# Kernel tuning notes

Measured on AMD Instinct MI355X. Metric: run time of the kernel, lower is better.

Reference implementation:

```python
import jax, jax.numpy as jnp
import numpy as np

# Dims: B INRs, N probe points, d_in=2 coords, hidden H, out D_OUT, proj P
B, N, D_IN, H, D_OUT, P = 128, 4096, 2, 128, 3, 128
W0_SIREN = 30.0  # SIREN frequency scale
LN_EPS = 1e-5


def setup_inputs() -> dict:
    key = jax.random.key(0)
    ks = jax.random.split(key, 12)
    sn = lambda k, shape, sc: (jax.random.normal(k, shape, dtype=jnp.float32) * sc)
    return {
        # per-sample SIREN params, torch layout: weight [b, in, out, 1], bias [b, out, 1]
        "w0": sn(ks[0], (B, D_IN, H, 1), 1.0 / D_IN),
        "w1": sn(ks[1], (B, H, H, 1), np.sqrt(6.0 / H) / W0_SIREN),
        "w2": sn(ks[2], (B, H, D_OUT, 1), np.sqrt(6.0 / H) / W0_SIREN),
        "b0": sn(ks[3], (B, H, 1), 0.1),
        "b1": sn(ks[4], (B, H, 1), 0.1),
        "b2": sn(ks[5], (B, D_OUT, 1), 0.1),
        # learned probe coordinates, initialized U[-1, 1) as in the module
        "inputs": jax.random.uniform(ks[6], (1, N, D_IN), dtype=jnp.float32, minval=-1.0, maxval=1.0),
        # projection (num_inputs -> proj_dim) + LayerNorm params, one per probed layer (4 total)
        "pw": sn(ks[7], (4, N, P), 1.0 / np.sqrt(N)),
        "pb": jnp.zeros((4, P), jnp.float32),
        "ln_g": jnp.ones((4, P), jnp.float32),
        "ln_b": jnp.zeros((4, P), jnp.float32),
    }


def _layernorm(x, g, b):
    m = jnp.mean(x, axis=-1, keepdims=True)
    v = jnp.mean(jnp.square(x - m), axis=-1, keepdims=True)
    return (x - m) * jax.lax.rsqrt(v + LN_EPS) * g + b


def reference(w0, w1, w2, b0, b1, b2, inputs, pw, pb, ln_g, ln_b):
    b = w0.shape[0]
    x = jnp.broadcast_to(inputs, (b,) + inputs.shape[1:])  # [b, n, d_in]

    def lin(h, W, bb):
        # per-sample linear: [b,n,i] @ [b,i,o] + [b,1,o]
        return jnp.einsum('bni,bio->bno', h, W[..., 0]) + bb[:, None, :, 0]

    h1 = jnp.sin(W0_SIREN * lin(x, w0, b0))   # [b, n, H]
    h2 = jnp.sin(W0_SIREN * lin(h1, w1, b1))  # [b, n, H]
    h3 = lin(h2, w2, b2)                      # [b, n, D_OUT] (last layer: no sine)
    feats = [x, h1, h2, h3]  # probe features per node layer (input coords + activations)

    outs = []
    for i, f in enumerate(feats):
        # permute to [b, dim_i, n], project n -> P, then LayerNorm over P
        z = jnp.einsum('bnd,np->bdp', f, pw[i]) + pb[i]
        outs.append(_layernorm(z, ln_g[i], ln_b[i]))
    return jnp.concatenate(outs, axis=1)  # [b, d_in + H + H + D_OUT, P]
```

## Files before the change

kernel.cpp:

```cpp
#include <hip/hip_runtime.h>
#include <hip/hip_bf16.h>


typedef unsigned short u16;
typedef __attribute__((ext_vector_type(8))) short short8;
typedef __attribute__((ext_vector_type(4))) short short4v;
typedef __attribute__((ext_vector_type(4))) float f32x4;
typedef __attribute__((ext_vector_type(4))) float float4v;

#define DEV __device__ __forceinline__

#define KSC 4.7746482927568605f

DEV float b2f(u16 h){ return __uint_as_float(((unsigned)h) << 16); }
DEV u16 f2b(float f){
  unsigned u = __float_as_uint(f);
  return (u16)((u + 0x7FFFu + ((u >> 16) & 1u)) >> 16);
}
DEV u16 f2b_hw(float f){
  __hip_bfloat16 h = __float2bfloat16(f);
  return __builtin_bit_cast(unsigned short, h);
}
DEV float sin_rev(float r){
#if __has_builtin(__builtin_amdgcn_sinf)
  return __builtin_amdgcn_sinf(r);
#else
  return __sinf(r * 6.283185307179586f);
#endif
}
template<int C> DEV float dpp_add(float x){
  int yi = __builtin_amdgcn_update_dpp(0, __float_as_int(x), C, 0xF, 0xF, true);
  return x + __int_as_float(yi);
}
DEV float sum16(float x){
  x = dpp_add<0x128>(x); x = dpp_add<0x124>(x);
  x = dpp_add<0x122>(x); x = dpp_add<0x121>(x);
  return x;
}

DEV int is_bf16_fmt(const void* lng){ return *(const unsigned*)lng == 0x3F803F80u; }
struct In {
  const float* f; const u16* h; int bf;
  DEV In(const void* p, int b_) : f((const float*)p), h((const u16*)p), bf(b_) {}
  DEV float at(size_t i) const { return bf ? b2f(h[i]) : f[i]; }
};

__global__ __launch_bounds__(256) void k_prep(const void* pwv, const void* inpv,
                                              const void* lngv,
                                              u16* __restrict__ pwT,
                                              float* __restrict__ xbuf){
  const int bf = is_bf16_fmt(lngv);
  const int t = threadIdx.x;
  if (blockIdx.x == 256){
    In inp(inpv, bf);
    for (int i = t; i < 8192; i += 256) xbuf[i] = inp.at(i);
    return;
  }
  In pw(pwv, bf);
  __shared__ u16 tile[64 * 129];
  const int layer = blockIdx.x >> 6;
  const int n0 = (blockIdx.x & 63) * 64;
  const size_t base = ((size_t)layer * 4096 + n0) * 128;
#pragma unroll
  for (int k = 0; k < 32; k++){
    int idx = k * 256 + t, n = idx >> 7, p = idx & 127;
    tile[n * 129 + p] = f2b(pw.at(base + (size_t)n * 128 + p));
  }
  __syncthreads();
  u16* dst = pwT + (size_t)layer * 128 * 4096 + n0;
#pragma unroll
  for (int k = 0; k < 32; k++){
    int idx = k * 256 + t, p = idx >> 6, n = idx & 63;
    dst[(size_t)p * 4096 + n] = tile[n * 129 + p];
  }
}

#define S_NK 136
#define S_T  40

template<bool PARTIAL>
__global__ __launch_bounds__(512, 2)
void k_main(const void* w0v, const void* w1v, const void* w2v,
            const void* b0v, const void* b1v, const void* b2v,
            const void* pbv, const void* lgv, const void* lbv,
            const u16* __restrict__ pwTg, const float* __restrict__ xbuf,
            float* __restrict__ outp, int TS){
  __shared__ __align__(16) u16 spw01[2][128 * S_T];
  __shared__ __align__(16) u16 spw23[2][2][128 * S_T];
  __shared__ __align__(16) u16 sh1nk[32 * S_NK];
  __shared__ __align__(16) u16 sh1T[128 * S_T];
  __shared__ __align__(16) u16 sh2T[2][128 * S_T];
  __shared__ __align__(16) u16 sxT[16 * S_T];
  __shared__ float sW2[512];
  __shared__ float sb2[4];
  __shared__ float sPB[512], sG[512], sBB[512];

  float* sP1 = (float*)sh1nk;
  float* sP2 = (float*)sh1T;
  float* sM  = (float*)sh2T;
  float* sI  = (float*)sh2T + 512;

  const int bf = is_bf16_fmt(lgv);
  In w0(w0v, bf), w1(w1v, bf), w2(w2v, bf), b0(b0v, bf), b1(b1v, bf),
     b2(b2v, bf), pb(pbv, bf), lg(lgv, bf), lb(lbv, bf);

  const int t = threadIdx.x;
  const int b = blockIdx.x & 127, sseg = blockIdx.x >> 7;
  const int lane = t & 63, wave = t >> 6, quad = lane >> 4, r16 = lane & 15;
  const int oo = wave * 16 + r16;

  if (t >= 256 && t < 384){
    int i = t - 256;
    sW2[i * 4 + 0] = w2.at(((size_t)b * 128 + i) * 3 + 0);
    sW2[i * 4 + 1] = w2.at(((size_t)b * 128 + i) * 3 + 1);
    sW2[i * 4 + 2] = w2.at(((size_t)b * 128 + i) * 3 + 2);
    sW2[i * 4 + 3] = 0.f;
  }
  if (t < 4) sb2[t] = (t < 3) ? b2.at(b * 3 + t) : 0.f;
  sPB[t] = pb.at(t); sG[t] = lg.at(t); sBB[t] = lb.at(t);
  for (int k = t; k < 16 * S_T; k += 512) sxT[k] = 0;

  const int p1n = t >> 4, p1hb = (t & 15) * 8;
  float w00[8], w01[8], b00[8];
#pragma unroll
  for (int j = 0; j < 8; j++){
    w00[j] = w0.at((size_t)b * 256 + p1hb + j) * KSC;
    w01[j] = w0.at((size_t)b * 256 + 128 + p1hb + j) * KSC;
    b00[j] = b0.at((size_t)b * 128 + p1hb + j) * KSC;
  }
  const int p2h = t & 127, p2nb = (t >> 7) * 8;
  const float q00 = w0.at((size_t)b * 256 + p2h) * KSC;
  const float q01 = w0.at((size_t)b * 256 + 128 + p2h) * KSC;
  const float qb0 = b0.at((size_t)b * 128 + p2h) * KSC;
  const float bias1k = b1.at((size_t)b * 128 + oo) * KSC;

  short8 w1f[4];
#pragma unroll
  for (int ks = 0; ks < 4; ks++){
#pragma unroll
    for (int j = 0; j < 8; j++)
      w1f[ks][j] = (short)f2b(w1.at((size_t)b * 16384 +
                                    (size_t)(ks * 32 + quad * 8 + j) * 128 + oo));
  }
  short8 a1s = {0,0,0,0,0,0,0,0};
  if (r16 == 0){
#pragma unroll
    for (int j = 0; j < 8; j++) a1s[j] = (short)0x3F80;
  }

  const int pwrow = t >> 2, pwc = t & 3;
  const u16* pwsrc = pwTg + (size_t)pwrow * 4096 + pwc * 8;
  const int pwdofs = pwrow * S_T + pwc * 8;
  const int bofs = oo * S_T + quad * 8;

  const f32x4 zz = {0.f,0.f,0.f,0.f};
  f32x4 az1[8], az2[8], ay[8], az0 = zz, az3 = zz;
#pragma unroll
  for (int i = 0; i < 8; i++){ az1[i] = zz; az2[i] = zz; ay[i] = zz; }

  const int n0first = sseg * TS * 32;
  short8 pwv[4];
#pragma unroll
  for (int L = 0; L < 4; L++)
    pwv[L] = *(const short8*)(pwsrc + (size_t)L * 524288 + n0first);
  float2 xp1 = *(const float2*)(xbuf + (size_t)(n0first + p1n) * 2);

  __syncthreads();

  int cb = 0;
  for (int nt = 0; nt < TS; nt++){
    const int n0 = (sseg * TS + nt) * 32;

    float4v xq[4];
#pragma unroll
    for (int q = 0; q < 4; q++)
      xq[q] = *(const float4v*)(xbuf + (size_t)(n0 + p2nb) * 2 + q * 4);
    *(short8*)&spw01[0][pwdofs] = pwv[0];
    *(short8*)&spw01[1][pwdofs] = pwv[1];
    *(short8*)&spw23[cb][0][pwdofs] = pwv[2];
    *(short8*)&spw23[cb][1][pwdofs] = pwv[3];
    if ((t & 15) == 0){
      sxT[p1n] = f2b(xp1.x);
      sxT[S_T + p1n] = f2b(xp1.y);
    }
    {
      short8 v;
#pragma unroll
      for (int j = 0; j < 8; j++){
        float a = fmaf(xp1.y, w01[j], fmaf(xp1.x, w00[j], b00[j]));
        a -= rintf(a);
        v[j] = (short)f2b_hw(sin_rev(a));
      }
      *(short8*)&sh1nk[p1n * S_NK + p1hb] = v;
    }
    {
      short8 v;
#pragma unroll
      for (int j = 0; j < 8; j++){
        float x0 = xq[j >> 1][(j & 1) * 2], x1 = xq[j >> 1][(j & 1) * 2 + 1];
        float a = fmaf(x1, q01, fmaf(x0, q00, qb0));
        a -= rintf(a);
        v[j] = (short)f2b_hw(sin_rev(a));
      }
      *(short8*)&sh1T[p2h * S_T + p2nb] = v;
    }
    if (nt){
      const u16* s2p  = sh2T[cb ^ 1];
      const short8 bb2 = *(const short8*)&spw23[cb ^ 1][0][bofs];
      const short8 bb3 = *(const short8*)&spw23[cb ^ 1][1][bofs];
#pragma unroll
      for (int mb = 0; mb < 8; mb++){
        short8 a = *(const short8*)&s2p[(mb * 16 + r16) * S_T + quad * 8];
        az2[mb] = __builtin_amdgcn_mfma_f32_16x16x32_bf16(a, bb2, az2[mb], 0, 0, 0);
        ay[mb]  = __builtin_amdgcn_mfma_f32_16x16x32_bf16(a, bb3, ay[mb], 0, 0, 0);
      }
    }
    __syncthreads();

    {
      const int nn = (nt + 1 < TS) ? nt + 1 : nt;
      const int n0n = (sseg * TS + nn) * 32;
      short8 pwn[4];
#pragma unroll
      for (int L = 0; L < 4; L++)
        pwn[L] = *(const short8*)(pwsrc + (size_t)L * 524288 + n0n);
      float2 xp1n = *(const float2*)(xbuf + (size_t)(n0n + p1n) * 2);

      f32x4 h0 = zz, h1a = zz;
#pragma unroll
      for (int ks = 0; ks < 4; ks++){
        h0  = __builtin_amdgcn_mfma_f32_16x16x32_bf16(
                *(short8*)&sh1nk[r16 * S_NK + ks * 32 + quad * 8], w1f[ks], h0, 0, 0, 0);
        h1a = __builtin_amdgcn_mfma_f32_16x16x32_bf16(
                *(short8*)&sh1nk[(16 + r16) * S_NK + ks * 32 + quad * 8], w1f[ks], h1a, 0, 0, 0);
      }
      az0 = __builtin_amdgcn_mfma_f32_16x16x32_bf16(
              *(short8*)&sxT[r16 * S_T + quad * 8], *(short8*)&spw01[0][bofs], az0, 0, 0, 0);
#pragma unroll
      for (int mb = 0; mb < 8; mb++)
        az1[mb] = __builtin_amdgcn_mfma_f32_16x16x32_bf16(
                    *(short8*)&sh1T[(mb * 16 + r16) * S_T + quad * 8],
                    *(short8*)&spw01[1][bofs], az1[mb], 0, 0, 0);
      az3 = __builtin_amdgcn_mfma_f32_16x16x32_bf16(a1s, *(short8*)&spw23[cb][1][bofs], az3, 0, 0, 0);
      {
        short4v v;
#pragma unroll
        for (int r = 0; r < 4; r++){
          float a = fmaf(h0[r], KSC, bias1k); a -= rintf(a);
          v[r] = (short)f2b_hw(sin_rev(a));
        }
        *(short4v*)&sh2T[cb][oo * S_T + quad * 4] = v;
#pragma unroll
        for (int r = 0; r < 4; r++){
          float a = fmaf(h1a[r], KSC, bias1k); a -= rintf(a);
          v[r] = (short)f2b_hw(sin_rev(a));
        }
        *(short4v*)&sh2T[cb][oo * S_T + 16 + quad * 4] = v;
      }

#pragma unroll
      for (int L = 0; L < 4; L++) pwv[L] = pwn[L];
      xp1 = xp1n;
    }
    __syncthreads();
    cb ^= 1;
  }

  {
    const u16* s2p  = sh2T[cb ^ 1];
    const short8 bb2 = *(const short8*)&spw23[cb ^ 1][0][bofs];
    const short8 bb3 = *(const short8*)&spw23[cb ^ 1][1][bofs];
#pragma unroll
    for (int mb = 0; mb < 8; mb++){
      short8 a = *(const short8*)&s2p[(mb * 16 + r16) * S_T + quad * 8];
      az2[mb] = __builtin_amdgcn_mfma_f32_16x16x32_bf16(a, bb2, az2[mb], 0, 0, 0);
      ay[mb]  = __builtin_amdgcn_mfma_f32_16x16x32_bf16(a, bb3, ay[mb], 0, 0, 0);
    }
  }

  const int p = oo;
  float S3 = (quad == 0) ? az3[0] : 0.f;
  S3 += __shfl_xor(S3, 16, 64); S3 += __shfl_xor(S3, 32, 64);
  float z3v[3];
#pragma unroll
  for (int d = 0; d < 3; d++){
    float a = 0.f;
#pragma unroll
    for (int mb = 0; mb < 8; mb++)
#pragma unroll
      for (int r = 0; r < 4; r++)
        a = fmaf(sW2[(mb * 16 + quad * 4 + r) * 4 + d], ay[mb][r], a);
    a += __shfl_xor(a, 16, 64); a += __shfl_xor(a, 32, 64);
    z3v[d] = a + sb2[d] * S3;
  }

  if (PARTIAL){
    float* zp = outp + ((size_t)(sseg * 128 + b)) * 261 * 128;
    if (quad == 0){
#pragma unroll
      for (int r = 0; r < 2; r++) zp[(size_t)r * 128 + p] = az0[r];
#pragma unroll
      for (int d = 0; d < 3; d++) zp[(size_t)(258 + d) * 128 + p] = z3v[d];
    }
#pragma unroll
    for (int mb = 0; mb < 8; mb++)
#pragma unroll
      for (int r = 0; r < 4; r++){
        int drow = mb * 16 + quad * 4 + r;
        zp[(size_t)(2 + drow) * 128 + p]   = az1[mb][r];
        zp[(size_t)(130 + drow) * 128 + p] = az2[mb][r];
      }
    return;
  }

  const float pb0v = sPB[p],       pb1v = sPB[128 + p];
  const float pb2v = sPB[256 + p], pb3v = sPB[384 + p];

  auto rowsum = [&](float v, int row, bool wr){
    float s1 = sum16(v), s2 = sum16(v * v);
    if (wr && r16 == 0){ sP1[row * 8 + wave] = s1; sP2[row * 8 + wave] = s2; }
  };
#pragma unroll
  for (int r = 0; r < 2; r++) rowsum(az0[r] + pb0v, r, quad == 0);
#pragma unroll
  for (int mb = 0; mb < 8; mb++)
#pragma unroll
    for (int r = 0; r < 4; r++)
      rowsum(az1[mb][r] + pb1v, 2 + mb * 16 + quad * 4 + r, true);
#pragma unroll
  for (int mb = 0; mb < 8; mb++)
#pragma unroll
    for (int r = 0; r < 4; r++)
      rowsum(az2[mb][r] + pb2v, 130 + mb * 16 + quad * 4 + r, true);
#pragma unroll
  for (int d = 0; d < 3; d++) rowsum(z3v[d] + pb3v, 258 + d, quad == 0);
  __syncthreads();

  if (t < 261){
    float s1 = 0.f, s2 = 0.f;
#pragma unroll
    for (int w = 0; w < 8; w++){ s1 += sP1[t * 8 + w]; s2 += sP2[t * 8 + w]; }
    float m = s1 * (1.f / 128.f);
    float var = fmaf(-m, m, s2 * (1.f / 128.f));
    sM[t] = m;
    sI[t] = rsqrtf(fmaxf(var, 0.f) + 1e-5f);
  }
  __syncthreads();

  const size_t ob = (size_t)b * 261 * 128;
  auto emit = [&](float v, int row, int grp){
    outp[ob + (size_t)row * 128 + p] =
      (v - sM[row]) * sI[row] * sG[grp * 128 + p] + sBB[grp * 128 + p];
  };
  if (quad == 0){
#pragma unroll
    for (int r = 0; r < 2; r++) emit(az0[r] + pb0v, r, 0);
#pragma unroll
    for (int d = 0; d < 3; d++) emit(z3v[d] + pb3v, 258 + d, 3);
  }
#pragma unroll
  for (int mb = 0; mb < 8; mb++)
#pragma unroll
    for (int r = 0; r < 4; r++)
      emit(az1[mb][r] + pb1v, 2 + mb * 16 + quad * 4 + r, 1);
#pragma unroll
  for (int mb = 0; mb < 8; mb++)
#pragma unroll
    for (int r = 0; r < 4; r++)
      emit(az2[mb][r] + pb2v, 130 + mb * 16 + quad * 4 + r, 2);
}

__global__ __launch_bounds__(256)
void k_ln(const float* __restrict__ zp, const void* pbv, const void* lgv,
          const void* lbv, float* __restrict__ out, int split){
  const int bf = is_bf16_fmt(lgv);
  In pb(pbv, bf), lg(lgv, bf), lb(lbv, bf);
  const int lane = threadIdx.x & 63;
  const int row = blockIdx.x * 4 + (threadIdx.x >> 6);
  const int b = row / 261, d = row % 261;
  const int grp = (d < 2) ? 0 : (d < 130) ? 1 : (d < 258) ? 2 : 3;
  const int p0 = lane * 2;
  float v0 = pb.at(grp * 128 + p0), v1 = pb.at(grp * 128 + p0 + 1);
  for (int s2 = 0; s2 < split; s2++){
    const float* zr = zp + ((size_t)(s2 * 128 + b) * 261 + d) * 128;
    v0 += zr[p0]; v1 += zr[p0 + 1];
  }
  float s1 = v0 + v1, s2s = v0 * v0 + v1 * v1;
#pragma unroll
  for (int o = 1; o < 64; o <<= 1){
    s1 += __shfl_xor(s1, o, 64);
    s2s += __shfl_xor(s2s, o, 64);
  }
  float m = s1 * (1.f / 128.f);
  float var = fmaf(-m, m, s2s * (1.f / 128.f));
  float inv = rsqrtf(fmaxf(var, 0.f) + 1e-5f);
  float2 o2;
  o2.x = (v0 - m) * inv * lg.at(grp * 128 + p0)     + lb.at(grp * 128 + p0);
  o2.y = (v1 - m) * inv * lg.at(grp * 128 + p0 + 1) + lb.at(grp * 128 + p0 + 1);
  *(float2*)(out + (size_t)row * 128 + p0) = o2;
}

extern "C" void kernel_launch(void* const* d_in, const int* in_sizes, int n_in,
                              void* d_out, int out_size, void* d_ws, size_t ws_size,
                              hipStream_t stream){
  const void* w0  = d_in[0];
  const void* w1  = d_in[1];
  const void* w2  = d_in[2];
  const void* b0  = d_in[3];
  const void* b1  = d_in[4];
  const void* b2  = d_in[5];
  const void* inp = d_in[6];
  const void* pw  = d_in[7];
  const void* pb  = d_in[8];
  const void* lng = d_in[9];
  const void* lnb = d_in[10];
  float* out = (float*)d_out;

  u16* pwT    = (u16*)d_ws;
  float* xbuf = (float*)((char*)d_ws + (size_t)4 * 128 * 4096 * 2);
  const size_t zoff = (size_t)4 * 128 * 4096 * 2 + 8192 * 4;
  float* zp = (float*)((char*)d_ws + zoff);
  const size_t seg = (size_t)128 * 261 * 128 * 4;

  const int split = (ws_size >= zoff + 2 * seg) ? 2 : 1;

  k_prep<<<257, 256, 0, stream>>>(pw, inp, lng, pwT, xbuf);
  if (split == 2){
    k_main<true><<<256, 512, 0, stream>>>(w0, w1, w2, b0, b1, b2,
        pb, lng, lnb, pwT, xbuf, zp, 64);
    k_ln<<<(128 * 261) / 4, 256, 0, stream>>>(zp, pb, lng, lnb, out, 2);
  } else {
    k_main<false><<<128, 512, 0, stream>>>(w0, w1, w2, b0, b1, b2,
        pb, lng, lnb, pwT, xbuf, out, 128);
  }
}
```

Baseline: 226.7 us.

## Hoist batch-independent input and bias-sum projections into a separate precompute kernel

The probe coordinates are shared across the batch, so the layer-0 projection x·pw[0] is the same for every sample. The new k_zs kernel computes it once, together with the column sums of pw[3] used by the last-layer bias. The main kernel no longer streams pw[0] or issues the x and bias MFMAs per tile, which cuts one of four pw load streams and some shared-memory traffic; the LN kernels then read the precomputed sums. In exchange, k_zs runs one thread per output column over a serial 4096-element reduction on only two blocks, and that latency-bound launch sits on the critical path.

Result: slower. 622.8 us (+174.7%).

```diff
diff --git a/kernel.cpp b/kernel.cpp
--- a/kernel.cpp
+++ b/kernel.cpp
@@ -75,6 +75,34 @@
   }
 }
 
+__global__ __launch_bounds__(256)
+void k_zs(const void* pwv, const void* inpv, const void* lngv,
+          float* __restrict__ zs){
+  const int bf = is_bf16_fmt(lngv);
+  In pw(pwv, bf), inp(inpv, bf);
+  const int t = threadIdx.x;
+  if (blockIdx.x == 0){
+    const int d = t >> 7, p = t & 127;
+    float s = 0.f;
+    for (int n = 0; n < 4096; n += 4){
+#pragma unroll
+      for (int k = 0; k < 4; k++)
+        s = fmaf(inp.at((size_t)(n + k) * 2 + d),
+                 pw.at((size_t)(n + k) * 128 + p), s);
+    }
+    zs[d * 128 + p] = s;
+  } else if (t < 128){
+    const size_t base = (size_t)3 * 4096 * 128;
+    float s = 0.f;
+    for (int n = 0; n < 4096; n += 4){
+#pragma unroll
+      for (int k = 0; k < 4; k++)
+        s += pw.at(base + (size_t)(n + k) * 128 + t);
+    }
+    zs[256 + t] = s;
+  }
+}
+
 #define S_NK 136
 #define S_T  40
 
@@ -84,13 +112,13 @@
             const void* b0v, const void* b1v, const void* b2v,
             const void* pbv, const void* lgv, const void* lbv,
             const u16* __restrict__ pwTg, const float* __restrict__ xbuf,
+            const float* __restrict__ zs,
             float* __restrict__ outp, int TS){
-  __shared__ __align__(16) u16 spw01[2][128 * S_T];
+  __shared__ __align__(16) u16 spw1[128 * S_T];
   __shared__ __align__(16) u16 spw23[2][2][128 * S_T];
   __shared__ __align__(16) u16 sh1nk[32 * S_NK];
   __shared__ __align__(16) u16 sh1T[128 * S_T];
   __shared__ __align__(16) u16 sh2T[2][128 * S_T];
-  __shared__ __align__(16) u16 sxT[16 * S_T];
   __shared__ float sW2[512];
   __shared__ float sb2[4];
   __shared__ float sPB[512], sG[512], sBB[512];
@@ -118,7 +146,6 @@
   }
   if (t < 4) sb2[t] = (t < 3) ? b2.at(b * 3 + t) : 0.f;
   sPB[t] = pb.at(t); sG[t] = lg.at(t); sBB[t] = lb.at(t);
-  for (int k = t; k < 16 * S_T; k += 512) sxT[k] = 0;
 
   const int p1n = t >> 4, p1hb = (t & 15) * 8;
   float w00[8], w01[8], b00[8];
@@ -142,26 +169,21 @@
       w1f[ks][j] = (short)f2b(w1.at((size_t)b * 16384 +
                                     (size_t)(ks * 32 + quad * 8 + j) * 128 + oo));
   }
-  short8 a1s = {0,0,0,0,0,0,0,0};
-  if (r16 == 0){
-#pragma unroll
-    for (int j = 0; j < 8; j++) a1s[j] = (short)0x3F80;
-  }
-
-  const int pwrow = t >> 2, pwc = t & 3;
-  const u16* pwsrc = pwTg + (size_t)pwrow * 4096 + pwc * 8;
+
+  const int pwrow = t & 127, pwc = t >> 7;
+  const u16* pwsrc = pwTg + (size_t)524288 + (size_t)pwrow * 4096 + pwc * 8;
   const int pwdofs = pwrow * S_T + pwc * 8;
   const int bofs = oo * S_T + quad * 8;
 
   const f32x4 zz = {0.f,0.f,0.f,0.f};
-  f32x4 az1[8], az2[8], ay[8], az0 = zz, az3 = zz;
+  f32x4 az1[8], az2[8], ay[8];
 #pragma unroll
   for (int i = 0; i < 8; i++){ az1[i] = zz; az2[i] = zz; ay[i] = zz; }
 
   const int n0first = sseg * TS * 32;
-  short8 pwv[4];
-#pragma unroll
-  for (int L = 0; L < 4; L++)
+  short8 pwv[3];
+#pragma unroll
+  for (int L = 0; L < 3; L++)
     pwv[L] = *(const short8*)(pwsrc + (size_t)L * 524288 + n0first);
   float2 xp1 = *(const float2*)(xbuf + (size_t)(n0first + p1n) * 2);
 
@@ -175,14 +197,9 @@
 #pragma unroll
     for (int q = 0; q < 4; q++)
       xq[q] = *(const float4v*)(xbuf + (size_t)(n0 + p2nb) * 2 + q * 4);
-    *(short8*)&spw01[0][pwdofs] = pwv[0];
-    *(short8*)&spw01[1][pwdofs] = pwv[1];
-    *(short8*)&spw23[cb][0][pwdofs] = pwv[2];
-    *(short8*)&spw23[cb][1][pwdofs] = pwv[3];
-    if ((t & 15) == 0){
-      sxT[p1n] = f2b(xp1.x);
-      sxT[S_T + p1n] = f2b(xp1.y);
-    }
+    *(short8*)&spw1[pwdofs] = pwv[0];
+    *(short8*)&spw23[cb][0][pwdofs] = pwv[1];
+    *(short8*)&spw23[cb][1][pwdofs] = pwv[2];
     {
       short8 v;
 #pragma unroll
@@ -220,9 +237,9 @@
     {
       const int nn = (nt + 1 < TS) ? nt + 1 : nt;
       const int n0n = (sseg * TS + nn) * 32;
-      short8 pwn[4];
-#pragma unroll
-      for (int L = 0; L < 4; L++)
+      short8 pwn[3];
+#pragma unroll
+      for (int L = 0; L < 3; L++)
         pwn[L] = *(const short8*)(pwsrc + (size_t)L * 524288 + n0n);
       float2 xp1n = *(const float2*)(xbuf + (size_t)(n0n + p1n) * 2);
 
@@ -234,14 +251,11 @@
         h1a = __builtin_amdgcn_mfma_f32_16x16x32_bf16(
                 *(short8*)&sh1nk[(16 + r16) * S_NK + ks * 32 + quad * 8], w1f[ks], h1a, 0, 0, 0);
       }
-      az0 = __builtin_amdgcn_mfma_f32_16x16x32_bf16(
-              *(short8*)&sxT[r16 * S_T + quad * 8], *(short8*)&spw01[0][bofs], az0, 0, 0, 0);
 #pragma unroll
       for (int mb = 0; mb < 8; mb++)
         az1[mb] = __builtin_amdgcn_mfma_f32_16x16x32_bf16(
                     *(short8*)&sh1T[(mb * 16 + r16) * S_T + quad * 8],
-                    *(short8*)&spw01[1][bofs], az1[mb], 0, 0, 0);
-      az3 = __builtin_amdgcn_mfma_f32_16x16x32_bf16(a1s, *(short8*)&spw23[cb][1][bofs], az3, 0, 0, 0);
+                    *(short8*)&spw1[bofs], az1[mb], 0, 0, 0);
       {
         short4v v;
 #pragma unroll
@@ -259,7 +273,7 @@
       }
 
 #pragma unroll
-      for (int L = 0; L < 4; L++) pwv[L] = pwn[L];
+      for (int L = 0; L < 3; L++) pwv[L] = pwn[L];
       xp1 = xp1n;
     }
     __syncthreads();
@@ -279,8 +293,6 @@
   }
 
   const int p = oo;
-  float S3 = (quad == 0) ? az3[0] : 0.f;
-  S3 += __shfl_xor(S3, 16, 64); S3 += __shfl_xor(S3, 32, 64);
   float z3v[3];
 #pragma unroll
   for (int d = 0; d < 3; d++){
@@ -291,14 +303,17 @@
       for (int r = 0; r < 4; r++)
         a = fmaf(sW2[(mb * 16 + quad * 4 + r) * 4 + d], ay[mb][r], a);
     a += __shfl_xor(a, 16, 64); a += __shfl_xor(a, 32, 64);
-    z3v[d] = a + sb2[d] * S3;
+    z3v[d] = a;
+  }
+  if (!PARTIAL){
+    const float S3v = zs[256 + p];
+#pragma unroll
+    for (int d = 0; d < 3; d++) z3v[d] += sb2[d] * S3v;
   }
 
   if (PARTIAL){
     float* zp = outp + ((size_t)(sseg * 128 + b)) * 261 * 128;
     if (quad == 0){
-#pragma unroll
-      for (int r = 0; r < 2; r++) zp[(size_t)r * 128 + p] = az0[r];
 #pragma unroll
       for (int d = 0; d < 3; d++) zp[(size_t)(258 + d) * 128 + p] = z3v[d];
     }
@@ -321,8 +336,6 @@
     if (wr && r16 == 0){ sP1[row * 8 + wave] = s1; sP2[row * 8 + wave] = s2; }
   };
 #pragma unroll
-  for (int r = 0; r < 2; r++) rowsum(az0[r] + pb0v, r, quad == 0);
-#pragma unroll
   for (int mb = 0; mb < 8; mb++)
 #pragma unroll
     for (int r = 0; r < 4; r++)
@@ -336,7 +349,17 @@
   for (int d = 0; d < 3; d++) rowsum(z3v[d] + pb3v, 258 + d, quad == 0);
   __syncthreads();
 
-  if (t < 261){
+  if (t < 2){
+    float s1 = 0.f, s2 = 0.f;
+    for (int pp = 0; pp < 128; pp++){
+      float v = zs[t * 128 + pp] + sPB[pp];
+      s1 += v; s2 += v * v;
+    }
+    float m = s1 * (1.f / 128.f);
+    float var = fmaf(-m, m, s2 * (1.f / 128.f));
+    sM[t] = m;
+    sI[t] = rsqrtf(fmaxf(var, 0.f) + 1e-5f);
+  } else if (t < 261){
     float s1 = 0.f, s2 = 0.f;
 #pragma unroll
     for (int w = 0; w < 8; w++){ s1 += sP1[t * 8 + w]; s2 += sP2[t * 8 + w]; }
@@ -354,7 +377,7 @@
   };
   if (quad == 0){
 #pragma unroll
-    for (int r = 0; r < 2; r++) emit(az0[r] + pb0v, r, 0);
+    for (int r = 0; r < 2; r++) emit(zs[r * 128 + p] + pb0v, r, 0);
 #pragma unroll
     for (int d = 0; d < 3; d++) emit(z3v[d] + pb3v, 258 + d, 3);
   }
@@ -372,18 +395,29 @@
 
 __global__ __launch_bounds__(256)
 void k_ln(const float* __restrict__ zp, const void* pbv, const void* lgv,
-          const void* lbv, float* __restrict__ out, int split){
+          const void* lbv, const void* b2v, const float* __restrict__ zs,
+          float* __restrict__ out, int split){
   const int bf = is_bf16_fmt(lgv);
-  In pb(pbv, bf), lg(lgv, bf), lb(lbv, bf);
+  In pb(pbv, bf), lg(lgv, bf), lb(lbv, bf), b2(b2v, bf);
   const int lane = threadIdx.x & 63;
   const int row = blockIdx.x * 4 + (threadIdx.x >> 6);
   const int b = row / 261, d = row % 261;
   const int grp = (d < 2) ? 0 : (d < 130) ? 1 : (d < 258) ? 2 : 3;
   const int p0 = lane * 2;
   float v0 = pb.at(grp * 128 + p0), v1 = pb.at(grp * 128 + p0 + 1);
-  for (int s2 = 0; s2 < split; s2++){
-    const float* zr = zp + ((size_t)(s2 * 128 + b) * 261 + d) * 128;
-    v0 += zr[p0]; v1 += zr[p0 + 1];
+  if (d < 2){
+    v0 += zs[d * 128 + p0];
+    v1 += zs[d * 128 + p0 + 1];
+  } else {
+    for (int s2 = 0; s2 < split; s2++){
+      const float* zr = zp + ((size_t)(s2 * 128 + b) * 261 + d) * 128;
+      v0 += zr[p0]; v1 += zr[p0 + 1];
+    }
+    if (d >= 258){
+      float bb = b2.at((size_t)b * 3 + (d - 258));
+      v0 = fmaf(bb, zs[256 + p0], v0);
+      v1 = fmaf(bb, zs[256 + p0 + 1], v1);
+    }
   }
   float s1 = v0 + v1, s2s = v0 * v0 + v1 * v1;
 #pragma unroll
@@ -418,19 +452,21 @@
 
   u16* pwT    = (u16*)d_ws;
   float* xbuf = (float*)((char*)d_ws + (size_t)4 * 128 * 4096 * 2);
-  const size_t zoff = (size_t)4 * 128 * 4096 * 2 + 8192 * 4;
+  float* zs   = (float*)((char*)d_ws + (size_t)4 * 128 * 4096 * 2 + 8192 * 4);
+  const size_t zoff = (size_t)4 * 128 * 4096 * 2 + 8192 * 4 + 2048;
   float* zp = (float*)((char*)d_ws + zoff);
   const size_t seg = (size_t)128 * 261 * 128 * 4;
 
   const int split = (ws_size >= zoff + 2 * seg) ? 2 : 1;
 
   k_prep<<<257, 256, 0, stream>>>(pw, inp, lng, pwT, xbuf);
+  k_zs<<<2, 256, 0, stream>>>(pw, inp, lng, zs);
   if (split == 2){
     k_main<true><<<256, 512, 0, stream>>>(w0, w1, w2, b0, b1, b2,
-        pb, lng, lnb, pwT, xbuf, zp, 64);
-    k_ln<<<(128 * 261) / 4, 256, 0, stream>>>(zp, pb, lng, lnb, out, 2);
+        pb, lng, lnb, pwT, xbuf, zs, zp, 64);
+    k_ln<<<(128 * 261) / 4, 256, 0, stream>>>(zp, pb, lng, lnb, b2, zs, out, 2);
   } else {
     k_main<false><<<128, 512, 0, stream>>>(w0, w1, w2, b0, b1, b2,
-        pb, lng, lnb, pwT, xbuf, out, 128);
-  }
-}
+        pb, lng, lnb, pwT, xbuf, zs, out, 128);
+  }
+}
```
